# Kernel tuning notes

Hardware: AMD Instinct MI355X
Metric: run time of the kernel (lower is better)

Reference implementation:

```python
import jax, jax.numpy as jnp
import numpy as np

B, H, S, DH = 2, 16, 2048, 64


def _decay_matrix(num_heads, seqlen):
    # RetNet per-head decay: gamma_h = 1 - 2^{-5-h}, D[h,n,m] = gamma_h^{n-m} for n>=m else 0
    h = np.arange(num_heads)
    gamma = 1.0 - 2.0 ** (-5.0 - h)  # [H]
    n = np.arange(seqlen)[:, None]
    m = np.arange(seqlen)[None, :]
    diff = (n - m).astype(np.float32)  # [S,S]
    D = np.where(diff >= 0, gamma[:, None, None] ** diff[None, :, :], 0.0)
    D = np.nan_to_num(D, nan=0.0)
    return jnp.asarray(D, dtype=jnp.float32)


def setup_inputs() -> dict:
    key = jax.random.key(0)
    kq, kk, kv = jax.random.split(key, 3)
    Q = jax.random.normal(kq, (B, H, S, DH), dtype=jnp.float32)
    K = jax.random.normal(kk, (B, H, S, DH), dtype=jnp.float32)
    V = jax.random.normal(kv, (B, H, S, DH), dtype=jnp.float32)
    D = _decay_matrix(H, S)  # [H,S,S]
    return {"Q": Q, "K": K, "V": V, "D": D}


def reference(Q, K, V, D):
    # scores = Q @ K^T : [B,H,S,S]
    scores = jnp.einsum("bhqd,bhkd->bhqk", Q, K)
    # retention: elementwise decay mask (no softmax), broadcast D over batch
    MSR = scores * D[None, :, :, :]
    out = jnp.einsum("bhqk,bhkd->bhqd", MSR, V)
    return (out, MSR)
```

## Files before the change

kernel.cpp:

```cpp
#include <hip/hip_runtime.h>
#include <hip/hip_bf16.h>
#include <math.h>

#define S_LEN 2048
#define DHEAD 64
#define NHEADS 16
#define NBATCH 2
#define TM 64
#define TN 64
#define CHUNK 8
#define LDSS 68
#define NTHR 256

typedef __attribute__((ext_vector_type(4))) float f32x4;
typedef __attribute__((ext_vector_type(4))) short s16x4;
typedef __attribute__((ext_vector_type(8))) short s16x8;

static __device__ __forceinline__ short f2bf(float f) {
    union { float f; unsigned u; } x; x.f = f;
    unsigned r = (x.u + 0x7fffu + ((x.u >> 16) & 1u)) >> 16;
    return (short)r;
}

static __device__ __forceinline__ s16x8 ld_frag(const short* p) {
    const s16x4* p4 = (const s16x4*)p;
    s16x4 lo = p4[0], hi = p4[1];
    s16x8 r;
    r[0]=lo[0]; r[1]=lo[1]; r[2]=lo[2]; r[3]=lo[3];
    r[4]=hi[0]; r[5]=hi[1]; r[6]=hi[2]; r[7]=hi[3];
    return r;
}

__global__ void zero_out_kernel(float* __restrict__ out) {
    size_t i = (size_t)blockIdx.x * NTHR + threadIdx.x;
    ((f32x4*)out)[i] = (f32x4){0.f, 0.f, 0.f, 0.f};
}

__global__ __launch_bounds__(NTHR, 4)
void retnet_fused(const float* __restrict__ Q, const float* __restrict__ K,
                  const float* __restrict__ V, float* __restrict__ out,
                  float* __restrict__ msr) {
    __shared__ short Qs[TM * LDSS];
    __shared__ short Ks[TN * LDSS];
    __shared__ short Vts[DHEAD * LDSS];
    __shared__ short Ps[TM * LDSS];

    const int t   = blockIdx.x;
    const int ch  = blockIdx.y;
    const int bh  = blockIdx.z;
    const int h   = bh & (NHEADS - 1);
    const int tid = threadIdx.x;
    const int w   = tid >> 6;
    const int l   = tid & 63;
    const int n0  = t * TM;

    const int cbeg   = ch * CHUNK;
    const int cend   = cbeg + CHUNK;
    const int mt_end = (t + 1 < cend) ? (t + 1) : cend;

    const float* Qp = Q + (size_t)bh * S_LEN * DHEAD;
    const float* Kp = K + (size_t)bh * S_LEN * DHEAD;
    const float* Vp = V + (size_t)bh * S_LEN * DHEAD;
    float* outp = out + (size_t)bh * S_LEN * DHEAD;
    float* msrp = msr + (size_t)bh * S_LEN * S_LEN;

    const float gamma = 1.0f - exp2f(-5.0f - (float)h);
    const float log2g = (float)log2((double)gamma);

    const int colid = l & 15;
    const int quad  = l >> 4;
    const int arow  = (w << 4) + colid;
    const int k0    = quad << 3;

    if (cbeg < mt_end) {
        #pragma unroll
        for (int p = 0; p < 4; ++p) {
            int idx = p * NTHR + tid;
            int row = idx >> 4;
            int c4  = (idx & 15) << 2;
            f32x4 q = *(const f32x4*)(Qp + (n0 + row) * DHEAD + c4);
            s16x4 qb; qb[0]=f2bf(q[0]); qb[1]=f2bf(q[1]); qb[2]=f2bf(q[2]); qb[3]=f2bf(q[3]);
            *(s16x4*)(&Qs[row * LDSS + c4]) = qb;
        }

        f32x4 accO[4];
        #pragma unroll
        for (int c = 0; c < 4; ++c) accO[c] = (f32x4){0.f,0.f,0.f,0.f};

        for (int mt = cbeg; mt < mt_end; ++mt) {
            const int m0 = mt * TN;
            __syncthreads();

            #pragma unroll
            for (int p = 0; p < 4; ++p) {
                int idx = p * NTHR + tid;
                int row = idx >> 4;
                int c4  = (idx & 15) << 2;
                f32x4 k = *(const f32x4*)(Kp + (m0 + row) * DHEAD + c4);
                s16x4 kb; kb[0]=f2bf(k[0]); kb[1]=f2bf(k[1]); kb[2]=f2bf(k[2]); kb[3]=f2bf(k[3]);
                *(s16x4*)(&Ks[row * LDSS + c4]) = kb;
            }
            #pragma unroll
            for (int p = 0; p < 4; ++p) {
                int d0 = ((p << 2) + w) << 2;
                f32x4 v = *(const f32x4*)(Vp + (m0 + l) * DHEAD + d0);
                Vts[(d0 + 0) * LDSS + l] = f2bf(v[0]);
                Vts[(d0 + 1) * LDSS + l] = f2bf(v[1]);
                Vts[(d0 + 2) * LDSS + l] = f2bf(v[2]);
                Vts[(d0 + 3) * LDSS + l] = f2bf(v[3]);
            }
            __syncthreads();

            f32x4 accS[4];
            #pragma unroll
            for (int c = 0; c < 4; ++c) accS[c] = (f32x4){0.f,0.f,0.f,0.f};
            #pragma unroll
            for (int kc = 0; kc < 2; ++kc) {
                s16x8 a = ld_frag(&Qs[arow * LDSS + (kc << 5) + k0]);
                #pragma unroll
                for (int c = 0; c < 4; ++c) {
                    s16x8 b = ld_frag(&Ks[((c << 4) + colid) * LDSS + (kc << 5) + k0]);
                    accS[c] = __builtin_amdgcn_mfma_f32_16x16x32_bf16(a, b, accS[c], 0, 0, 0);
                }
            }

            #pragma unroll
            for (int c = 0; c < 4; ++c) {
                int mloc = (c << 4) + colid;
                int m = m0 + mloc;
                #pragma unroll
                for (int r = 0; r < 4; ++r) {
                    int nloc = (w << 4) + (quad << 2) + r;
                    int n = n0 + nloc;
                    int delta = n - m;
                    float dec = (delta >= 0) ? exp2f((float)delta * log2g) : 0.0f;
                    float val = accS[c][r] * dec;
                    msrp[(size_t)n * S_LEN + m] = val;
                    Ps[nloc * LDSS + mloc] = f2bf(val);
                }
            }
            __syncthreads();

            #pragma unroll
            for (int kc = 0; kc < 2; ++kc) {
                s16x8 a = ld_frag(&Ps[arow * LDSS + (kc << 5) + k0]);
                #pragma unroll
                for (int c = 0; c < 4; ++c) {
                    s16x8 b = ld_frag(&Vts[((c << 4) + colid) * LDSS + (kc << 5) + k0]);
                    accO[c] = __builtin_amdgcn_mfma_f32_16x16x32_bf16(a, b, accO[c], 0, 0, 0);
                }
            }
        }

        #pragma unroll
        for (int c = 0; c < 4; ++c) {
            int d = (c << 4) + colid;
            #pragma unroll
            for (int r = 0; r < 4; ++r) {
                int nloc = (w << 4) + (quad << 2) + r;
                unsafeAtomicAdd(&outp[(n0 + nloc) * DHEAD + d], accO[c][r]);
            }
        }
    }

    const int zbeg = (cbeg > t + 1) ? cbeg : (t + 1);
    if (zbeg < cend) {
        const int z0 = zbeg << 6;
        const int z1 = cend << 6;
        const f32x4 z4 = (f32x4){0.f,0.f,0.f,0.f};
        #pragma unroll
        for (int rp = 0; rp < 4; ++rp) {
            float* rowp = msrp + (size_t)(n0 + (rp << 4) + (tid >> 4)) * S_LEN;
            for (int cc = z0 + ((tid & 15) << 2); cc < z1; cc += 64) {
                *(f32x4*)(rowp + cc) = z4;
            }
        }
    }
}

extern "C" void kernel_launch(void* const* d_in, const int* in_sizes, int n_in,
                              void* d_out, int out_size, void* d_ws, size_t ws_size,
                              hipStream_t stream) {
    const float* Q = (const float*)d_in[0];
    const float* K = (const float*)d_in[1];
    const float* V = (const float*)d_in[2];
    float* out = (float*)d_out;
    float* msr = out + (size_t)NBATCH * NHEADS * S_LEN * DHEAD;

    const int o_elems = NBATCH * NHEADS * S_LEN * DHEAD;
    zero_out_kernel<<<o_elems / 4 / NTHR, NTHR, 0, stream>>>(out);

    dim3 grid(S_LEN / TM, S_LEN / TN / CHUNK, NBATCH * NHEADS);
    retnet_fused<<<grid, NTHR, 0, stream>>>(Q, K, V, out, msr);
}
```

Measured before the change: 789.7 us.

## Prefetch K/V into registers, factor decay, vectorize LDS fragments, nontemporal MSR stores

Loads the next K/V tile into registers while the current tile is staged in LDS, so global-load latency overlaps with compute. The LDS row stride goes from 68 to 72 so MFMA fragments can be read with single 16-byte loads instead of two 8-byte loads. The per-element exp2 for the decay becomes one exp2 per column times precomputed gamma powers, with causal masking applied only on the diagonal tile. MSR and zero-fill writes use nontemporal stores. The barrier between the P write and the PV MFMA is dropped, since each wave only reads its own rows. The costs are extra registers for the prefetched tiles and slightly different rounding in the decay factors.

```diff
diff --git a/kernel.cpp b/kernel.cpp
--- a/kernel.cpp
+++ b/kernel.cpp
@@ -9,7 +9,7 @@
 #define TM 64
 #define TN 64
 #define CHUNK 8
-#define LDSS 68
+#define LDSS 72
 #define NTHR 256
 
 typedef __attribute__((ext_vector_type(4))) float f32x4;
@@ -20,15 +20,6 @@
     union { float f; unsigned u; } x; x.f = f;
     unsigned r = (x.u + 0x7fffu + ((x.u >> 16) & 1u)) >> 16;
     return (short)r;
-}
-
-static __device__ __forceinline__ s16x8 ld_frag(const short* p) {
-    const s16x4* p4 = (const s16x4*)p;
-    s16x4 lo = p4[0], hi = p4[1];
-    s16x8 r;
-    r[0]=lo[0]; r[1]=lo[1]; r[2]=lo[2]; r[3]=lo[3];
-    r[4]=hi[0]; r[5]=hi[1]; r[6]=hi[2]; r[7]=hi[3];
-    return r;
 }
 
 __global__ void zero_out_kernel(float* __restrict__ out) {
@@ -66,11 +57,14 @@
 
     const float gamma = 1.0f - exp2f(-5.0f - (float)h);
     const float log2g = (float)log2((double)gamma);
+    const float g2 = gamma * gamma;
+    const float g3 = g2 * gamma;
 
     const int colid = l & 15;
     const int quad  = l >> 4;
     const int arow  = (w << 4) + colid;
     const int k0    = quad << 3;
+    const int nrow0 = (w << 4) + (quad << 2);
 
     if (cbeg < mt_end) {
         #pragma unroll
@@ -83,6 +77,19 @@
             *(s16x4*)(&Qs[row * LDSS + c4]) = qb;
         }
 
+        const int srow = tid >> 4;
+        const int sc4  = (tid & 15) << 2;
+
+        f32x4 kreg[4], vreg[4];
+        {
+            const int m0 = cbeg * TN;
+            #pragma unroll
+            for (int p = 0; p < 4; ++p) {
+                kreg[p] = *(const f32x4*)(Kp + (size_t)(m0 + (p << 4) + srow) * DHEAD + sc4);
+                vreg[p] = *(const f32x4*)(Vp + (size_t)(m0 + l) * DHEAD + (((p << 2) + w) << 2));
+            }
+        }
+
         f32x4 accO[4];
         #pragma unroll
         for (int c = 0; c < 4; ++c) accO[c] = (f32x4){0.f,0.f,0.f,0.f};
@@ -93,21 +100,25 @@
 
             #pragma unroll
             for (int p = 0; p < 4; ++p) {
-                int idx = p * NTHR + tid;
-                int row = idx >> 4;
-                int c4  = (idx & 15) << 2;
-                f32x4 k = *(const f32x4*)(Kp + (m0 + row) * DHEAD + c4);
-                s16x4 kb; kb[0]=f2bf(k[0]); kb[1]=f2bf(k[1]); kb[2]=f2bf(k[2]); kb[3]=f2bf(k[3]);
-                *(s16x4*)(&Ks[row * LDSS + c4]) = kb;
+                s16x4 kb; kb[0]=f2bf(kreg[p][0]); kb[1]=f2bf(kreg[p][1]);
+                          kb[2]=f2bf(kreg[p][2]); kb[3]=f2bf(kreg[p][3]);
+                *(s16x4*)(&Ks[((p << 4) + srow) * LDSS + sc4]) = kb;
             }
             #pragma unroll
             for (int p = 0; p < 4; ++p) {
                 int d0 = ((p << 2) + w) << 2;
-                f32x4 v = *(const f32x4*)(Vp + (m0 + l) * DHEAD + d0);
-                Vts[(d0 + 0) * LDSS + l] = f2bf(v[0]);
-                Vts[(d0 + 1) * LDSS + l] = f2bf(v[1]);
-                Vts[(d0 + 2) * LDSS + l] = f2bf(v[2]);
-                Vts[(d0 + 3) * LDSS + l] = f2bf(v[3]);
+                Vts[(d0 + 0) * LDSS + l] = f2bf(vreg[p][0]);
+                Vts[(d0 + 1) * LDSS + l] = f2bf(vreg[p][1]);
+                Vts[(d0 + 2) * LDSS + l] = f2bf(vreg[p][2]);
+                Vts[(d0 + 3) * LDSS + l] = f2bf(vreg[p][3]);
+            }
+            if (mt + 1 < mt_end) {
+                const int m0n = m0 + TN;
+                #pragma unroll
+                for (int p = 0; p < 4; ++p) {
+                    kreg[p] = *(const f32x4*)(Kp + (size_t)(m0n + (p << 4) + srow) * DHEAD + sc4);
+                    vreg[p] = *(const f32x4*)(Vp + (size_t)(m0n + l) * DHEAD + (((p << 2) + w) << 2));
+                }
             }
             __syncthreads();
 
@@ -116,37 +127,46 @@
             for (int c = 0; c < 4; ++c) accS[c] = (f32x4){0.f,0.f,0.f,0.f};
             #pragma unroll
             for (int kc = 0; kc < 2; ++kc) {
-                s16x8 a = ld_frag(&Qs[arow * LDSS + (kc << 5) + k0]);
+                s16x8 a = *(const s16x8*)(&Qs[arow * LDSS + (kc << 5) + k0]);
                 #pragma unroll
                 for (int c = 0; c < 4; ++c) {
-                    s16x8 b = ld_frag(&Ks[((c << 4) + colid) * LDSS + (kc << 5) + k0]);
+                    s16x8 b = *(const s16x8*)(&Ks[((c << 4) + colid) * LDSS + (kc << 5) + k0]);
                     accS[c] = __builtin_amdgcn_mfma_f32_16x16x32_bf16(a, b, accS[c], 0, 0, 0);
                 }
             }
 
+            float dec0[4];
             #pragma unroll
             for (int c = 0; c < 4; ++c) {
-                int mloc = (c << 4) + colid;
-                int m = m0 + mloc;
-                #pragma unroll
-                for (int r = 0; r < 4; ++r) {
-                    int nloc = (w << 4) + (quad << 2) + r;
-                    int n = n0 + nloc;
-                    int delta = n - m;
-                    float dec = (delta >= 0) ? exp2f((float)delta * log2g) : 0.0f;
-                    float val = accS[c][r] * dec;
-                    msrp[(size_t)n * S_LEN + m] = val;
-                    Ps[nloc * LDSS + mloc] = f2bf(val);
-                }
-            }
-            __syncthreads();
+                int delta0 = (n0 + nrow0) - (m0 + (c << 4) + colid);
+                dec0[c] = exp2f((float)delta0 * log2g);
+            }
+            const bool diag = (mt == t);
+
+            #pragma unroll
+            for (int r = 0; r < 4; ++r) {
+                const float gr = (r == 0) ? 1.0f : (r == 1) ? gamma : (r == 2) ? g2 : g3;
+                const int nloc = nrow0 + r;
+                float* rowp = msrp + (size_t)(n0 + nloc) * S_LEN + (m0 + colid);
+                short* prow = &Ps[nloc * LDSS + colid];
+                #pragma unroll
+                for (int c = 0; c < 4; ++c) {
+                    float val = accS[c][r] * (dec0[c] * gr);
+                    if (diag) {
+                        int delta = (n0 + nloc) - (m0 + (c << 4) + colid);
+                        if (delta < 0) val = 0.0f;
+                    }
+                    __builtin_nontemporal_store(val, rowp + (c << 4));
+                    prow[c << 4] = f2bf(val);
+                }
+            }
 
             #pragma unroll
             for (int kc = 0; kc < 2; ++kc) {
-                s16x8 a = ld_frag(&Ps[arow * LDSS + (kc << 5) + k0]);
+                s16x8 a = *(const s16x8*)(&Ps[arow * LDSS + (kc << 5) + k0]);
                 #pragma unroll
                 for (int c = 0; c < 4; ++c) {
-                    s16x8 b = ld_frag(&Vts[((c << 4) + colid) * LDSS + (kc << 5) + k0]);
+                    s16x8 b = *(const s16x8*)(&Vts[((c << 4) + colid) * LDSS + (kc << 5) + k0]);
                     accO[c] = __builtin_amdgcn_mfma_f32_16x16x32_bf16(a, b, accO[c], 0, 0, 0);
                 }
             }
@@ -157,7 +177,7 @@
             int d = (c << 4) + colid;
             #pragma unroll
             for (int r = 0; r < 4; ++r) {
-                int nloc = (w << 4) + (quad << 2) + r;
+                int nloc = nrow0 + r;
                 unsafeAtomicAdd(&outp[(n0 + nloc) * DHEAD + d], accO[c][r]);
             }
         }
@@ -172,7 +192,7 @@
         for (int rp = 0; rp < 4; ++rp) {
             float* rowp = msrp + (size_t)(n0 + (rp << 4) + (tid >> 4)) * S_LEN;
             for (int cc = z0 + ((tid & 15) << 2); cc < z1; cc += 64) {
-                *(f32x4*)(rowp + cc) = z4;
+                __builtin_nontemporal_store(z4, (f32x4*)(rowp + cc));
             }
         }
     }
```

Measured after the change: 779.5 us. No clear change (-1.3%).
